# Kernel optimization log

Measured on AMD Instinct MI355X. Metric: run time of the kernel, lower is better.

The kernel has to match this reference:

```python
import jax, jax.numpy as jnp
import numpy as np

D_MODEL, D_STATE, HEAD_DIM, EXPAND, K, N_GROUPS = 1024, 128, 64, 2, 4, 1
D_INNER = EXPAND * D_MODEL            # 2048
N_HEADS = D_INNER // HEAD_DIM         # 32
D_PROJ = 2 * D_INNER + 2 * N_GROUPS * D_STATE + N_HEADS  # 4384
EPS = 1e-6


def setup_inputs() -> dict:
    key = jax.random.key(0)
    ks = jax.random.split(key, 8)
    B, L = 2, 2048
    x = jax.random.normal(ks[0], (B, L, D_MODEL), dtype=jnp.float32)
    norm_w = jnp.ones((D_MODEL,), jnp.float32)
    in_proj_w = jax.random.normal(ks[1], (D_PROJ, D_MODEL), jnp.float32) * (D_MODEL ** -0.5)
    conv_w = jax.random.normal(ks[2], (D_INNER, 1, K), jnp.float32) * (K ** -0.5)
    conv_b = jnp.zeros((D_INNER,), jnp.float32)
    A_log = jnp.log(jax.random.uniform(ks[3], (N_HEADS,)) * 15.0 + 1.0)
    D = jnp.ones((N_HEADS,), jnp.float32)
    dt_bias = jnp.log(jax.random.uniform(ks[4], (N_HEADS,)) * 0.099 + 0.001)
    out_proj_w = jax.random.normal(ks[5], (D_MODEL, D_INNER), jnp.float32) * (D_INNER ** -0.5)
    return {"x": x, "norm_w": norm_w, "in_proj_w": in_proj_w, "conv_w": conv_w,
            "conv_b": conv_b, "A_log": A_log, "D": D, "dt_bias": dt_bias,
            "out_proj_w": out_proj_w}


def _silu(v):
    return v * jax.nn.sigmoid(v)


def reference(x, norm_w, in_proj_w, conv_w, conv_b, A_log, D, dt_bias, out_proj_w):
    Bsz, L, _ = x.shape
    residual = x
    # RMSNorm (pre-norm)
    xn = x * jax.lax.rsqrt(jnp.mean(x * x, axis=-1, keepdims=True) + EPS) * norm_w
    proj = xn @ in_proj_w.T                                     # (B, L, D_PROJ)
    # split fused projection -> (z, x_ssm, B, C, dt_raw)
    i = 0
    z = proj[..., i:i + D_INNER]; i += D_INNER
    x_ssm = proj[..., i:i + D_INNER]; i += D_INNER
    bc = N_GROUPS * D_STATE
    Bm = proj[..., i:i + bc].reshape(Bsz, L, N_GROUPS, D_STATE); i += bc
    Cm = proj[..., i:i + bc].reshape(Bsz, L, N_GROUPS, D_STATE); i += bc
    dt_raw = proj[..., i:i + N_HEADS]
    # causal depthwise conv1d (torch pad=K-1 then slice [:L] == left-pad K-1)
    xc = jnp.transpose(x_ssm, (0, 2, 1))                        # (B, D_INNER, L)
    xc = jax.lax.conv_general_dilated(
        xc, conv_w, window_strides=(1,), padding=[(K - 1, 0)],
        dimension_numbers=("NCH", "OIH", "NCH"), feature_group_count=D_INNER)
    xc = xc + conv_b[None, :, None]
    x_conv = _silu(jnp.transpose(xc, (0, 2, 1)))                # (B, L, D_INNER)
    # discretisation
    dt = jax.nn.softplus(dt_raw + dt_bias)                      # (B, L, H)
    dA = jnp.exp(-jnp.exp(A_log)[None, None, :] * dt)           # (B, L, H)
    x_heads = x_conv.reshape(Bsz, L, N_HEADS, HEAD_DIM)
    dt_x = dt[..., None] * x_heads                              # (B, L, H, P)
    group_idx = jnp.arange(N_HEADS) // (N_HEADS // N_GROUPS)
    Bg = Bm[:, :, group_idx, :]                                 # (B, L, H, N)
    Cg = Cm[:, :, group_idx, :]
    # sequential selective scan over time via lax.scan (fp32 state)
    def step(h, inp):
        dA_t, dtx_t, B_t, C_t = inp                             # (B,H),(B,H,P),(B,H,N),(B,H,N)
        h = h * dA_t[..., None, None] + dtx_t[..., None] * B_t[:, :, None, :]
        y_t = jnp.einsum("bhpn,bhn->bhp", h, C_t)
        return h, y_t
    h0 = jnp.zeros((Bsz, N_HEADS, HEAD_DIM, D_STATE), jnp.float32)
    xs = (jnp.moveaxis(dA, 1, 0).astype(jnp.float32),
          jnp.moveaxis(dt_x, 1, 0).astype(jnp.float32),
          jnp.moveaxis(Bg, 1, 0).astype(jnp.float32),
          jnp.moveaxis(Cg, 1, 0).astype(jnp.float32))
    _, y = jax.lax.scan(step, h0, xs)                           # y: (L, B, H, P)
    y = jnp.moveaxis(y, 0, 1).astype(x.dtype)                   # (B, L, H, P)
    y = y + D[None, None, :, None] * x_heads
    y = y.reshape(Bsz, L, D_INNER) * _silu(z)                   # gated output
    return residual + y @ out_proj_w.T
```

## Files before the change

kernel.cpp:

```cpp
#include <hip/hip_runtime.h>
#include <math.h>

#define B_SZ     2
#define L_SEQ    2048
#define DM       1024
#define DP       4384
#define PS       4480
#define DI       2048
#define NH       32
#define HD       64
#define DS       128
#define M_ROWS   (B_SZ * L_SEQ)
#define QCH      64
#define NC       (L_SEQ / QCH)

typedef __bf16 bf16x8 __attribute__((ext_vector_type(8)));
typedef __bf16 bf16x4 __attribute__((ext_vector_type(4)));
typedef float  f32x4  __attribute__((ext_vector_type(4)));

__device__ __forceinline__ void gload16(const void* g, void* l) {
    __builtin_amdgcn_global_load_lds(
        (const __attribute__((address_space(1))) unsigned int*)g,
        (__attribute__((address_space(3))) unsigned int*)l,
        16, 0, 0);
}

__global__ __launch_bounds__(256) void k_prep(const float* __restrict__ Wp,
                                              __bf16* __restrict__ Wpb,
                                              const float* __restrict__ x,
                                              const float* __restrict__ w,
                                              __bf16* __restrict__ xn) {
    int tid = threadIdx.x;
    if (blockIdx.x < 4384) {
        int i = blockIdx.x * 256 + tid;
        float4 v = ((const float4*)Wp)[i];
        bf16x4 o = { (__bf16)v.x, (__bf16)v.y, (__bf16)v.z, (__bf16)v.w };
        ((bf16x4*)Wpb)[i] = o;
        return;
    }
    int row = blockIdx.x - 4384;
    const float4* x4 = (const float4*)(x + (long)row * DM);
    float4 v = x4[tid];
    float ss = v.x * v.x + v.y * v.y + v.z * v.z + v.w * v.w;
    #pragma unroll
    for (int off = 32; off > 0; off >>= 1) ss += __shfl_xor(ss, off, 64);
    __shared__ float sred[4];
    if ((tid & 63) == 0) sred[tid >> 6] = ss;
    __syncthreads();
    float tot = sred[0] + sred[1] + sred[2] + sred[3];
    float scale = rsqrtf(tot * (1.0f / (float)DM) + 1e-6f);
    const float4* w4 = (const float4*)w;
    float4 wv = w4[tid];
    bf16x4 o = { (__bf16)(v.x * scale * wv.x), (__bf16)(v.y * scale * wv.y),
                 (__bf16)(v.z * scale * wv.z), (__bf16)(v.w * scale * wv.w) };
    ((bf16x4*)(xn + (long)row * DM))[tid] = o;
}

__global__ __launch_bounds__(256) void k_gemm_bf(const __bf16* __restrict__ A,
                                                 const __bf16* __restrict__ W,
                                                 const float* __restrict__ resid,
                                                 float* __restrict__ Cf,
                                                 __bf16* __restrict__ Cb,
                                                 float* __restrict__ Dt,
                                                 int Nw, int K, int ldc) {
    __shared__ __align__(16) __bf16 As[2][128 * 64];
    __shared__ __align__(16) __bf16 Bs[2][128 * 64];
    int t = threadIdx.x;

    int gx = gridDim.x;
    int nwg = gx * gridDim.y;
    int orig = blockIdx.y * gx + blockIdx.x;
    int wgid = (nwg & 7) ? orig : ((orig & 7) * (nwg >> 3) + (orig >> 3));
    int bx = wgid % gx, by = wgid / gx;
    int bm = by * 128, bn = bx * 128;

    int lane = t & 63, w = t >> 6;

    int rl = lane >> 3;
    int lc = (lane & 7) ^ rl;
    int rbase = w * 32 + rl;
    const __bf16* Agp[4];
    const __bf16* Wgp[4];
    #pragma unroll
    for (int i = 0; i < 4; i++) {
        Agp[i] = A + (long)(bm + rbase + i * 8) * K + lc * 8;
        int rb = bn + rbase + i * 8; if (rb >= Nw) rb = Nw - 1;
        Wgp[i] = W + (long)rb * K + lc * 8;
    }

    int wm = (w & 1) * 64, wn = (w >> 1) * 64;
    int ln = lane & 15;
    int q  = lane >> 4;

    f32x4 acc[4][4] = {};

    int nst = K >> 6;

    #pragma unroll
    for (int i = 0; i < 4; i++) {
        gload16(Agp[i], As[0] + (w * 4 + i) * 512);
        gload16(Wgp[i], Bs[0] + (w * 4 + i) * 512);
    }

    int cur = 0;
    for (int s = 0; s < nst; ++s) {
        if (s + 1 < nst) {
            long k1 = (long)(s + 1) << 6;
            #pragma unroll
            for (int i = 0; i < 4; i++) {
                gload16(Agp[i] + k1, As[cur ^ 1] + (w * 4 + i) * 512);
                gload16(Wgp[i] + k1, Bs[cur ^ 1] + (w * 4 + i) * 512);
            }
            asm volatile("s_waitcnt vmcnt(8)" ::: "memory");
        } else {
            asm volatile("s_waitcnt vmcnt(0)" ::: "memory");
        }
        __builtin_amdgcn_sched_barrier(0);
        __builtin_amdgcn_s_barrier();
        __builtin_amdgcn_sched_barrier(0);

        const __bf16* Asc = As[cur];
        const __bf16* Bsc = Bs[cur];
        __builtin_amdgcn_s_setprio(1);
        #pragma unroll
        for (int h = 0; h < 2; h++) {
            int ch = (4 * h + q);
            int koff = ((ch ^ (ln & 7)) << 3);
            bf16x8 af[4], bfr[4];
            #pragma unroll
            for (int i = 0; i < 4; i++)
                af[i]  = *(const bf16x8*)(Asc + (wm + ln + i * 16) * 64 + koff);
            #pragma unroll
            for (int j = 0; j < 4; j++)
                bfr[j] = *(const bf16x8*)(Bsc + (wn + ln + j * 16) * 64 + koff);
            #pragma unroll
            for (int i = 0; i < 4; i++)
                #pragma unroll
                for (int j = 0; j < 4; j++)
                    acc[i][j] = __builtin_amdgcn_mfma_f32_16x16x32_bf16(
                                    af[i], bfr[j], acc[i][j], 0, 0, 0);
        }
        __builtin_amdgcn_s_setprio(0);
        __builtin_amdgcn_sched_barrier(0);
        __builtin_amdgcn_s_barrier();
        __builtin_amdgcn_sched_barrier(0);
        cur ^= 1;
    }

    int colbase = bn + wn + ln;
    #pragma unroll
    for (int i = 0; i < 4; i++) {
        #pragma unroll
        for (int r = 0; r < 4; r++) {
            int m = bm + wm + i * 16 + (lane >> 4) * 4 + r;
            long off = (long)m * ldc + colbase;
            #pragma unroll
            for (int j = 0; j < 4; j++) {
                float v = acc[i][j][r];
                if (Cb != nullptr) {
                    Cb[off + j * 16] = (__bf16)v;
                    if (Dt != nullptr) {
                        int col = colbase + j * 16;
                        if (col >= 4352 && col < 4384)
                            Dt[(long)m * 32 + (col - 4352)] = v;
                    }
                } else {
                    if (resid != nullptr) v += resid[off + j * 16];
                    Cf[off + j * 16] = v;
                }
            }
        }
    }
}

__global__ __launch_bounds__(256) void k_chunk(const __bf16* __restrict__ projb,
                                               const float* __restrict__ dtraw,
                                               const float* __restrict__ cw,
                                               const float* __restrict__ cb,
                                               const float* __restrict__ A_log,
                                               const float* __restrict__ dt_bias,
                                               const float* __restrict__ Dv,
                                               float* __restrict__ clog,
                                               __bf16* __restrict__ yssm,
                                               float* __restrict__ Sloc) {
    int blk = blockIdx.x;
    int c  = blk & 31;
    int hh = (blk >> 5) & 31;
    int b  = blk >> 10;
    int tid = threadIdx.x;
    long rowbase = (long)b * L_SEQ + c * QCH;

    __shared__ __align__(16) __bf16 sB[64 * 136];
    __shared__ __align__(16) __bf16 sU[128 * 72];
    __shared__ __align__(16) __bf16 sXT[64 * 72];
    __shared__ __align__(16) __bf16 sXCM[67 * 72];
    __shared__ __align__(16) __bf16 sXCo[64 * 72];
    __shared__ float sCW[256];
    __shared__ float sCB[64];
    __shared__ float sclog[64];
    __shared__ float sdt[64];
    __shared__ float sw[64];

    #pragma unroll
    for (int j = 0; j < 4; j++) {
        int off = j * 256 + tid;
        int t  = off >> 4;
        int n8 = (off & 15) * 8;
        const __bf16* pr = projb + (rowbase + t) * (long)PS;
        *(bf16x8*)&sB[t * 136 + n8] = *(const bf16x8*)(pr + 4096 + n8);
        *(bf16x8*)&sU[t * 136 + n8] = *(const bf16x8*)(pr + 4224 + n8);
    }
    #pragma unroll
    for (int j = 0; j < 3; j++) {
        int off = j * 256 + tid;
        if (off < 536) {
            int ss = off >> 3;
            int p8 = (off & 7) * 8;
            bf16x8 xv;
            #pragma unroll
            for (int k = 0; k < 8; k++) xv[k] = (__bf16)0.0f;
            if (c > 0 || ss >= 3)
                xv = *(const bf16x8*)(projb + (rowbase + ss - 3) * (long)PS + DI + hh * HD + p8);
            *(bf16x8*)&sXCM[ss * 72 + p8] = xv;
        }
    }
    sCW[tid] = cw[hh * 256 + tid];
    if (tid < 64) sCB[tid] = cb[hh * 64 + tid];

    if (tid < 64) {
        float xr = dtraw[(rowbase + tid) * 32 + hh] + dt_bias[hh];
        float dt = (xr > 20.0f) ? xr : log1pf(expf(xr));
        float la = -expf(A_log[hh]);
        float v = la * dt;
        #pragma unroll
        for (int off = 1; off < 64; off <<= 1) {
            float u = __shfl_up(v, off, 64);
            if (tid >= off) v += u;
        }
        sdt[tid] = dt;
        sclog[tid] = v;
        clog[(rowbase + tid) * NH + hh] = v;
    }
    __syncthreads();

    {
        int p8 = (tid & 7) * 8;
        float wreg[8][4], breg[8];
        #pragma unroll
        for (int e = 0; e < 8; e++) {
            breg[e] = sCB[p8 + e];
            #pragma unroll
            for (int j = 0; j < 4; j++) wreg[e][j] = sCW[(p8 + e) * 4 + j];
        }
        #pragma unroll
        for (int i = 0; i < 2; i++) {
            int s = i * 32 + (tid >> 3);
            bf16x8 r0 = *(const bf16x8*)&sXCM[(s + 0) * 72 + p8];
            bf16x8 r1 = *(const bf16x8*)&sXCM[(s + 1) * 72 + p8];
            bf16x8 r2 = *(const bf16x8*)&sXCM[(s + 2) * 72 + p8];
            bf16x8 r3 = *(const bf16x8*)&sXCM[(s + 3) * 72 + p8];
            float dts = sdt[s];
            bf16x8 oc;
            #pragma unroll
            for (int e = 0; e < 8; e++) {
                float acc = breg[e];
                acc = fmaf(wreg[e][0], (float)r0[e], acc);
                acc = fmaf(wreg[e][1], (float)r1[e], acc);
                acc = fmaf(wreg[e][2], (float)r2[e], acc);
                acc = fmaf(wreg[e][3], (float)r3[e], acc);
                float xc = acc / (1.0f + expf(-acc));
                oc[e] = (__bf16)xc;
                sXT[(p8 + e) * 72 + s] = (__bf16)(dts * xc);
            }
            *(bf16x8*)&sXCo[s * 72 + p8] = oc;
        }
    }
    if (tid < 64) sw[tid] = expf(sclog[63] - sclog[tid]);
    __syncthreads();

    int lane = tid & 63, w = tid >> 6;
    int ln = lane & 15;
    int quad = lane >> 4;
    int kc = quad * 8;

    bf16x8 caf[4];
    #pragma unroll
    for (int k0 = 0; k0 < 4; k0++)
        caf[k0] = *(const bf16x8*)&sU[(16 * w + ln) * 136 + kc + k0 * 32];
    f32x4 g[4] = {};
    #pragma unroll
    for (int j = 0; j < 4; j++)
        #pragma unroll
        for (int k0 = 0; k0 < 4; k0++) {
            bf16x8 bf_ = *(const bf16x8*)&sB[(16 * j + ln) * 136 + kc + k0 * 32];
            g[j] = __builtin_amdgcn_mfma_f32_16x16x32_bf16(caf[k0], bf_, g[j], 0, 0, 0);
        }

    {
        int trow = 16 * w + quad * 4;
        #pragma unroll
        for (int r = 0; r < 4; r++) {
            int t = trow + r;
            float ct = sclog[t];
            #pragma unroll
            for (int j = 0; j < 4; j++) {
                int s = 16 * j + ln;
                float v = (s <= t) ? g[j][r] * expf(ct - sclog[s]) : 0.0f;
                sXCM[t * 72 + s] = (__bf16)v;
            }
        }
    }
    __syncthreads();

    #pragma unroll
    for (int j = 0; j < 4; j++) {
        int s  = tid & 63;
        int n8 = (j * 4 + (tid >> 6)) * 8;
        bf16x8 v = *(const bf16x8*)&sB[s * 136 + n8];
        #pragma unroll
        for (int k = 0; k < 8; k++) sU[(n8 + k) * 72 + s] = v[k];
    }

    {
        float Dh = Dv[hh];
        bf16x8 maf[2];
        #pragma unroll
        for (int k0 = 0; k0 < 2; k0++)
            maf[k0] = *(const bf16x8*)&sXCM[(16 * w + ln) * 72 + kc + k0 * 32];
        f32x4 y[4] = {};
        #pragma unroll
        for (int j = 0; j < 4; j++)
            #pragma unroll
            for (int k0 = 0; k0 < 2; k0++) {
                bf16x8 xf = *(const bf16x8*)&sXT[(16 * j + ln) * 72 + kc + k0 * 32];
                y[j] = __builtin_amdgcn_mfma_f32_16x16x32_bf16(maf[k0], xf, y[j], 0, 0, 0);
            }
        #pragma unroll
        for (int j = 0; j < 4; j++)
            #pragma unroll
            for (int r = 0; r < 4; r++) {
                int t = 16 * w + quad * 4 + r;
                int p = 16 * j + ln;
                float v = y[j][r] + Dh * (float)sXCo[t * 72 + p];
                yssm[(rowbase + t) * DI + hh * HD + p] = (__bf16)v;
            }
    }
    __syncthreads();

    {
        bf16x8 xaf[2];
        #pragma unroll
        for (int k0 = 0; k0 < 2; k0++) {
            bf16x8 raw = *(const bf16x8*)&sXT[(16 * w + ln) * 72 + kc + k0 * 32];
            bf16x8 sc;
            #pragma unroll
            for (int jj = 0; jj < 8; jj++) {
                int s = kc + k0 * 32 + jj;
                sc[jj] = (__bf16)((float)raw[jj] * sw[s]);
            }
            xaf[k0] = sc;
        }
        f32x4 sacc[8] = {};
        #pragma unroll
        for (int j = 0; j < 8; j++)
            #pragma unroll
            for (int k0 = 0; k0 < 2; k0++) {
                bf16x8 btf = *(const bf16x8*)&sU[(16 * j + ln) * 72 + kc + k0 * 32];
                sacc[j] = __builtin_amdgcn_mfma_f32_16x16x32_bf16(xaf[k0], btf, sacc[j], 0, 0, 0);
            }
        long sbase = ((long)(b * NH + hh) * NC + c) * (HD * DS);
        #pragma unroll
        for (int j = 0; j < 8; j++)
            #pragma unroll
            for (int r = 0; r < 4; r++) {
                int p = 16 * w + quad * 4 + r;
                int n = 16 * j + ln;
                Sloc[sbase + p * DS + n] = sacc[j][r];
            }
    }
}

__global__ __launch_bounds__(256) void k_carry_f2b(float* __restrict__ Sloc,
                                                   const float* __restrict__ clog,
                                                   const float* __restrict__ Wo,
                                                   __bf16* __restrict__ Wob) {
    int bid = blockIdx.x;
    int tid = threadIdx.x;
    if (bid >= 2048) {
        int i = (bid - 2048) * 256 + tid;
        float4 v = ((const float4*)Wo)[i];
        bf16x4 o = { (__bf16)v.x, (__bf16)v.y, (__bf16)v.z, (__bf16)v.w };
        ((bf16x4*)Wob)[i] = o;
        return;
    }
    int idx = bid * 256 + tid;
    int n  = idx & 127;
    int p  = (idx >> 7) & 63;
    int hh = (idx >> 13) & 31;
    int b  = idx >> 18;
    long base = ((long)(b * NH + hh) * NC) * (HD * DS) + p * DS + n;
    float T = 0.0f;
    for (int c = 0; c < NC; c++) {
        float lam = expf(clog[((long)b * L_SEQ + c * QCH + QCH - 1) * NH + hh]);
        long a = base + (long)c * (HD * DS);
        float S = Sloc[a];
        Sloc[a] = T;
        T = fmaf(T, lam, S);
    }
}

__global__ __launch_bounds__(256, 2) void k_fix(const __bf16* __restrict__ projb,
                                                const float* __restrict__ Sloc,
                                                const float* __restrict__ clog,
                                                const __bf16* __restrict__ yb,
                                                __bf16* __restrict__ yg) {
    int blk = blockIdx.x;
    int c  = blk & 31;
    int hh = (blk >> 5) & 31;
    int b  = blk >> 10;

    __shared__ __align__(16) __bf16 sC[64 * 136];
    __shared__ __align__(16) __bf16 sH[64 * 136];
    __shared__ float sP[64];

    int tid = threadIdx.x;
    long hbase = ((long)(b * NH + hh) * NC + c) * (HD * DS);
    long rowbase = (long)b * L_SEQ + c * QCH;

    #pragma unroll
    for (int j = 0; j < 4; j++) {
        int off = j * 256 + tid;
        int t  = off >> 4;
        int n8 = (off & 15) * 8;
        *(bf16x8*)&sC[t * 136 + n8] =
            *(const bf16x8*)(projb + (rowbase + t) * (long)PS + 4224 + n8);
    }
    #pragma unroll
    for (int j = 0; j < 8; j++) {
        int off = j * 256 + tid;
        int p  = off >> 5;
        int n4 = (off & 31) * 4;
        float4 hv = *(const float4*)&Sloc[hbase + (long)off * 4];
        bf16x4 hb = {(__bf16)hv.x, (__bf16)hv.y, (__bf16)hv.z, (__bf16)hv.w};
        *(bf16x4*)&sH[p * 136 + n4] = hb;
    }
    if (tid < 64) sP[tid] = expf(clog[(rowbase + tid) * NH + hh]);
    __syncthreads();

    int lane = tid & 63, w = tid >> 6;
    int ln = lane & 15;
    int quad = lane >> 4;
    int kc = quad * 8;

    bf16x8 caf[4];
    #pragma unroll
    for (int k0 = 0; k0 < 4; k0++)
        caf[k0] = *(const bf16x8*)&sC[(16 * w + ln) * 136 + kc + k0 * 32];
    f32x4 acc4[4] = {};
    #pragma unroll
    for (int j = 0; j < 4; j++)
        #pragma unroll
        for (int k0 = 0; k0 < 4; k0++) {
            bf16x8 hf = *(const bf16x8*)&sH[(16 * j + ln) * 136 + kc + k0 * 32];
            acc4[j] = __builtin_amdgcn_mfma_f32_16x16x32_bf16(caf[k0], hf, acc4[j], 0, 0, 0);
        }

    #pragma unroll
    for (int j = 0; j < 4; j++)
        #pragma unroll
        for (int r = 0; r < 4; r++) {
            int t = 16 * w + quad * 4 + r;
            int p = 16 * j + ln;
            long row = rowbase + t;
            long yoff = row * DI + hh * HD + p;
            float pm = sP[t];
            float z = (float)projb[row * (long)PS + hh * HD + p];
            float o = ((float)yb[yoff] + pm * acc4[j][r]) * (z / (1.0f + expf(-z)));
            yg[yoff] = (__bf16)o;
        }
}

extern "C" void kernel_launch(void* const* d_in, const int* in_sizes, int n_in,
                              void* d_out, int out_size, void* d_ws, size_t ws_size,
                              hipStream_t stream) {
    const float* x       = (const float*)d_in[0];
    const float* norm_w  = (const float*)d_in[1];
    const float* Wp      = (const float*)d_in[2];
    const float* cw      = (const float*)d_in[3];
    const float* cb      = (const float*)d_in[4];
    const float* A_log   = (const float*)d_in[5];
    const float* Dv      = (const float*)d_in[6];
    const float* dt_bias = (const float*)d_in[7];
    const float* Wo      = (const float*)d_in[8];
    float* out = (float*)d_out;

    float* ws     = (float*)d_ws;
    __bf16* projb = (__bf16*)ws;
    float* dtraw  = ws    + 9175040;
    float* clog   = dtraw + 131072;
    float* ybh    = clog  + 131072;
    float* ybf    = ybh   + 4194304;
    float* wob_s  = ybf   + 4194304;
    float* U      = wob_s + 1048576;

    __bf16* xnb  = (__bf16*)U;
    __bf16* Wpb  = (__bf16*)(U + 2097152);
    float*  Sloc = U;
    __bf16* Wob  = (__bf16*)wob_s;
    __bf16* ybb  = (__bf16*)ybf;
    __bf16* yb   = (__bf16*)ybh;

    k_prep<<<4384 + M_ROWS, 256, 0, stream>>>(Wp, Wpb, x, norm_w, xnb);
    {
        dim3 g(PS / 128, M_ROWS / 128);
        k_gemm_bf<<<g, 256, 0, stream>>>(xnb, Wpb, nullptr, nullptr, projb,
                                         dtraw, DP, DM, PS);
    }

    k_chunk<<<B_SZ * NH * NC, 256, 0, stream>>>(projb, dtraw, cw, cb, A_log,
                                                dt_bias, Dv, clog, yb, Sloc);
    k_carry_f2b<<<4096, 256, 0, stream>>>(Sloc, clog, Wo, Wob);
    k_fix<<<B_SZ * NH * NC, 256, 0, stream>>>(projb, Sloc, clog, yb, ybb);

    {
        dim3 g(DM / 128, M_ROWS / 128);
        k_gemm_bf<<<g, 256, 0, stream>>>(ybb, Wob, x, out, nullptr, nullptr,
                                         DM, DI, DM);
    }
}
```

Baseline: 296.7 us.

## Store chunk SSM states in bf16 and add a syncthreads-based out_proj GEMM variant

The per-chunk SSM states (Sloc) are now written by k_chunk, rewritten by the carry kernel and read by k_fix in bf16 instead of fp32. This roughly halves the memory traffic of that large intermediate. The carry kernel processes two state elements per thread with bf16x2 accesses, so it needs half as many blocks, while keeping the running carry in fp32. The GEMM is templated on its scheduling mode: the in_proj keeps the manual vmcnt, s_barrier and setprio pipeline, and the out_proj uses plain __syncthreads. Rounding the per-chunk states to bf16 before they are accumulated adds some numerical error, and the __syncthreads variant may reduce load/compute overlap in the out_proj GEMM.

```diff
diff --git a/kernel.cpp b/kernel.cpp
--- a/kernel.cpp
+++ b/kernel.cpp
@@ -16,6 +16,7 @@
 
 typedef __bf16 bf16x8 __attribute__((ext_vector_type(8)));
 typedef __bf16 bf16x4 __attribute__((ext_vector_type(4)));
+typedef __bf16 bf16x2 __attribute__((ext_vector_type(2)));
 typedef float  f32x4  __attribute__((ext_vector_type(4)));
 
 __device__ __forceinline__ void gload16(const void* g, void* l) {
@@ -56,6 +57,7 @@
     ((bf16x4*)(xn + (long)row * DM))[tid] = o;
 }
 
+template<int SCHED>
 __global__ __launch_bounds__(256) void k_gemm_bf(const __bf16* __restrict__ A,
                                                  const __bf16* __restrict__ W,
                                                  const float* __restrict__ resid,
@@ -101,6 +103,7 @@
         gload16(Agp[i], As[0] + (w * 4 + i) * 512);
         gload16(Wgp[i], Bs[0] + (w * 4 + i) * 512);
     }
+    if (SCHED == 0) __syncthreads();
 
     int cur = 0;
     for (int s = 0; s < nst; ++s) {
@@ -111,17 +114,21 @@
                 gload16(Agp[i] + k1, As[cur ^ 1] + (w * 4 + i) * 512);
                 gload16(Wgp[i] + k1, Bs[cur ^ 1] + (w * 4 + i) * 512);
             }
-            asm volatile("s_waitcnt vmcnt(8)" ::: "memory");
+            if (SCHED == 1)
+                asm volatile("s_waitcnt vmcnt(8)" ::: "memory");
         } else {
-            asm volatile("s_waitcnt vmcnt(0)" ::: "memory");
-        }
-        __builtin_amdgcn_sched_barrier(0);
-        __builtin_amdgcn_s_barrier();
-        __builtin_amdgcn_sched_barrier(0);
+            if (SCHED == 1)
+                asm volatile("s_waitcnt vmcnt(0)" ::: "memory");
+        }
+        if (SCHED == 1) {
+            __builtin_amdgcn_sched_barrier(0);
+            __builtin_amdgcn_s_barrier();
+            __builtin_amdgcn_sched_barrier(0);
+            __builtin_amdgcn_s_setprio(1);
+        }
 
         const __bf16* Asc = As[cur];
         const __bf16* Bsc = Bs[cur];
-        __builtin_amdgcn_s_setprio(1);
         #pragma unroll
         for (int h = 0; h < 2; h++) {
             int ch = (4 * h + q);
@@ -140,10 +147,14 @@
                     acc[i][j] = __builtin_amdgcn_mfma_f32_16x16x32_bf16(
                                     af[i], bfr[j], acc[i][j], 0, 0, 0);
         }
-        __builtin_amdgcn_s_setprio(0);
-        __builtin_amdgcn_sched_barrier(0);
-        __builtin_amdgcn_s_barrier();
-        __builtin_amdgcn_sched_barrier(0);
+        if (SCHED == 1) {
+            __builtin_amdgcn_s_setprio(0);
+            __builtin_amdgcn_sched_barrier(0);
+            __builtin_amdgcn_s_barrier();
+            __builtin_amdgcn_sched_barrier(0);
+        } else {
+            __syncthreads();
+        }
         cur ^= 1;
     }
 
@@ -182,7 +193,7 @@
                                                const float* __restrict__ Dv,
                                                float* __restrict__ clog,
                                                __bf16* __restrict__ yssm,
-                                               float* __restrict__ Sloc) {
+                                               __bf16* __restrict__ Sloc) {
     int blk = blockIdx.x;
     int c  = blk & 31;
     int hh = (blk >> 5) & 31;
@@ -375,42 +386,45 @@
             for (int r = 0; r < 4; r++) {
                 int p = 16 * w + quad * 4 + r;
                 int n = 16 * j + ln;
-                Sloc[sbase + p * DS + n] = sacc[j][r];
-            }
-    }
-}
-
-__global__ __launch_bounds__(256) void k_carry_f2b(float* __restrict__ Sloc,
+                Sloc[sbase + p * DS + n] = (__bf16)sacc[j][r];
+            }
+    }
+}
+
+__global__ __launch_bounds__(256) void k_carry_f2b(__bf16* __restrict__ Sloc,
                                                    const float* __restrict__ clog,
                                                    const float* __restrict__ Wo,
                                                    __bf16* __restrict__ Wob) {
     int bid = blockIdx.x;
     int tid = threadIdx.x;
-    if (bid >= 2048) {
-        int i = (bid - 2048) * 256 + tid;
+    if (bid >= 1024) {
+        int i = (bid - 1024) * 256 + tid;
         float4 v = ((const float4*)Wo)[i];
         bf16x4 o = { (__bf16)v.x, (__bf16)v.y, (__bf16)v.z, (__bf16)v.w };
         ((bf16x4*)Wob)[i] = o;
         return;
     }
     int idx = bid * 256 + tid;
-    int n  = idx & 127;
-    int p  = (idx >> 7) & 63;
-    int hh = (idx >> 13) & 31;
-    int b  = idx >> 18;
-    long base = ((long)(b * NH + hh) * NC) * (HD * DS) + p * DS + n;
-    float T = 0.0f;
+    int n2 = idx & 63;
+    int p  = (idx >> 6) & 63;
+    int hh = (idx >> 12) & 31;
+    int b  = idx >> 17;
+    long base = ((long)(b * NH + hh) * NC) * (HD * DS) + p * DS + n2 * 2;
+    float T0 = 0.0f, T1 = 0.0f;
     for (int c = 0; c < NC; c++) {
         float lam = expf(clog[((long)b * L_SEQ + c * QCH + QCH - 1) * NH + hh]);
         long a = base + (long)c * (HD * DS);
-        float S = Sloc[a];
-        Sloc[a] = T;
-        T = fmaf(T, lam, S);
+        bf16x2 Sv = *(const bf16x2*)&Sloc[a];
+        float S0 = (float)Sv[0], S1 = (float)Sv[1];
+        bf16x2 Tv = { (__bf16)T0, (__bf16)T1 };
+        *(bf16x2*)&Sloc[a] = Tv;
+        T0 = fmaf(T0, lam, S0);
+        T1 = fmaf(T1, lam, S1);
     }
 }
 
 __global__ __launch_bounds__(256, 2) void k_fix(const __bf16* __restrict__ projb,
-                                                const float* __restrict__ Sloc,
+                                                const __bf16* __restrict__ Sloc,
                                                 const float* __restrict__ clog,
                                                 const __bf16* __restrict__ yb,
                                                 __bf16* __restrict__ yg) {
@@ -436,13 +450,11 @@
             *(const bf16x8*)(projb + (rowbase + t) * (long)PS + 4224 + n8);
     }
     #pragma unroll
-    for (int j = 0; j < 8; j++) {
+    for (int j = 0; j < 4; j++) {
         int off = j * 256 + tid;
-        int p  = off >> 5;
-        int n4 = (off & 31) * 4;
-        float4 hv = *(const float4*)&Sloc[hbase + (long)off * 4];
-        bf16x4 hb = {(__bf16)hv.x, (__bf16)hv.y, (__bf16)hv.z, (__bf16)hv.w};
-        *(bf16x4*)&sH[p * 136 + n4] = hb;
+        int p  = off >> 4;
+        int n8 = (off & 15) * 8;
+        *(bf16x8*)&sH[p * 136 + n8] = *(const bf16x8*)&Sloc[hbase + (long)off * 8];
     }
     if (tid < 64) sP[tid] = expf(clog[(rowbase + tid) * NH + hh]);
     __syncthreads();
@@ -505,7 +517,7 @@
 
     __bf16* xnb  = (__bf16*)U;
     __bf16* Wpb  = (__bf16*)(U + 2097152);
-    float*  Sloc = U;
+    __bf16* Sloc = (__bf16*)U;
     __bf16* Wob  = (__bf16*)wob_s;
     __bf16* ybb  = (__bf16*)ybf;
     __bf16* yb   = (__bf16*)ybh;
@@ -513,18 +525,18 @@
     k_prep<<<4384 + M_ROWS, 256, 0, stream>>>(Wp, Wpb, x, norm_w, xnb);
     {
         dim3 g(PS / 128, M_ROWS / 128);
-        k_gemm_bf<<<g, 256, 0, stream>>>(xnb, Wpb, nullptr, nullptr, projb,
-                                         dtraw, DP, DM, PS);
+        k_gemm_bf<1><<<g, 256, 0, stream>>>(xnb, Wpb, nullptr, nullptr, projb,
+                                            dtraw, DP, DM, PS);
     }
 
     k_chunk<<<B_SZ * NH * NC, 256, 0, stream>>>(projb, dtraw, cw, cb, A_log,
                                                 dt_bias, Dv, clog, yb, Sloc);
-    k_carry_f2b<<<4096, 256, 0, stream>>>(Sloc, clog, Wo, Wob);
+    k_carry_f2b<<<3072, 256, 0, stream>>>(Sloc, clog, Wo, Wob);
     k_fix<<<B_SZ * NH * NC, 256, 0, stream>>>(projb, Sloc, clog, yb, ybb);
 
     {
         dim3 g(DM / 128, M_ROWS / 128);
-        k_gemm_bf<<<g, 256, 0, stream>>>(ybb, Wob, x, out, nullptr, nullptr,
-                                         DM, DI, DM);
-    }
-}
+        k_gemm_bf<0><<<g, 256, 0, stream>>>(ybb, Wob, x, out, nullptr, nullptr,
+                                            DM, DI, DM);
+    }
+}
```

Result: faster. 279.0 us (-6.0%).
